# Kernel optimization log

Measured on AMD Instinct MI355X. Metric: run time of the kernel, lower is better.

Reference implementation:

```python
import jax, jax.numpy as jnp
import numpy as np

B, L, D_MODEL = 4, 2048, 2048
N_HEADS, HEAD_DIM = 16, 128
EPS = 1e-6


def _make_rope(key_unused, L, dim, base=10000.0):
    inv_freq = 1.0 / (base ** (np.arange(0, dim, 2, dtype=np.float32) / dim))  # [dim/2]
    t = np.arange(L, dtype=np.float32)
    freqs = np.outer(t, inv_freq)  # [L, dim/2]
    emb = np.concatenate([freqs, freqs], axis=-1)  # [L, dim]
    cos = np.broadcast_to(np.cos(emb)[None], (B, L, dim)).copy()
    sin = np.broadcast_to(np.sin(emb)[None], (B, L, dim)).copy()
    return jnp.asarray(cos), jnp.asarray(sin)


def setup_inputs() -> dict:
    key = jax.random.key(0)
    ks = jax.random.split(key, 8)
    s = 1.0 / np.sqrt(D_MODEL)
    x = jax.random.normal(ks[0], (B, L, D_MODEL), dtype=jnp.float32)
    cos_q, sin_q = _make_rope(None, L, HEAD_DIM)
    cos_k, sin_k = _make_rope(None, L, HEAD_DIM)
    Wq = jax.random.normal(ks[1], (D_MODEL, D_MODEL), dtype=jnp.float32) * s
    Wk = jax.random.normal(ks[2], (D_MODEL, D_MODEL), dtype=jnp.float32) * s
    Wv = jax.random.normal(ks[3], (D_MODEL, D_MODEL), dtype=jnp.float32) * s
    Wo = jax.random.normal(ks[4], (D_MODEL, D_MODEL), dtype=jnp.float32) * s
    q_gamma = jnp.ones((HEAD_DIM,), dtype=jnp.float32) + 0.02 * jax.random.normal(ks[5], (HEAD_DIM,), dtype=jnp.float32)
    k_gamma = jnp.ones((HEAD_DIM,), dtype=jnp.float32) + 0.02 * jax.random.normal(ks[6], (HEAD_DIM,), dtype=jnp.float32)
    return dict(x=x, cos_q=cos_q, sin_q=sin_q, cos_k=cos_k, sin_k=sin_k,
                Wq=Wq, Wk=Wk, Wv=Wv, Wo=Wo, q_gamma=q_gamma, k_gamma=k_gamma)


def _rms_norm(h, w):
    # T5-style RMSNorm over last dim (head_dim), variance in fp32
    var = jnp.mean(h.astype(jnp.float32) ** 2, axis=-1, keepdims=True)
    return w * (h * jax.lax.rsqrt(var + EPS))


def _rotate_half(x):
    d = x.shape[-1] // 2
    return jnp.concatenate([-x[..., d:], x[..., :d]], axis=-1)


def _apply_rope(x, cos, sin):
    # x: [B, L, H, Dh]; cos/sin: [B, L, Dh] -> broadcast over heads
    c = cos[:, :, None, :]
    s = sin[:, :, None, :]
    return x * c + _rotate_half(x) * s


def reference(x, cos_q, sin_q, cos_k, sin_k, Wq, Wk, Wv, Wo, q_gamma, k_gamma):
    Bx, Lx, _ = x.shape
    # QKV projections (Linear with weight [out, in]: y = x @ W.T)
    q = (x @ Wq.T).reshape(Bx, Lx, N_HEADS, HEAD_DIM)
    k = (x @ Wk.T).reshape(Bx, Lx, N_HEADS, HEAD_DIM)
    v = (x @ Wv.T).reshape(Bx, Lx, N_HEADS, HEAD_DIM)
    # per-head QK RMSNorm
    q = _rms_norm(q, q_gamma)
    k = _rms_norm(k, k_gamma)
    # dual RoPE
    q = _apply_rope(q, cos_q, sin_q)
    k = _apply_rope(k, cos_k, sin_k)
    # scaled dot-product attention (dense, no mask)
    scale = 1.0 / jnp.sqrt(jnp.asarray(HEAD_DIM, dtype=x.dtype))
    scores = jnp.einsum('blhd,bmhd->bhlm', q, k) * scale
    attn = jax.nn.softmax(scores, axis=-1)
    out = jnp.einsum('bhlm,bmhd->blhd', attn, v)
    out = out.reshape(Bx, Lx, N_HEADS * HEAD_DIM)
    return out @ Wo.T
```

## Files before the change

kernel.cpp:

```cpp
#include <hip/hip_runtime.h>
#include <stdint.h>

#define DM   2048
#define LSEQ 2048
#define NB   4
#define NH   16
#define HD   128
#define BL   (NB*LSEQ)

typedef unsigned short u16;
typedef short  short8 __attribute__((ext_vector_type(8)));
typedef float  f32x4  __attribute__((ext_vector_type(4)));
typedef float  f32x16 __attribute__((ext_vector_type(16)));

#define LOG2E 1.4426950408889634f

__device__ __forceinline__ float bf2f(u16 v) {
    union { unsigned u; float f; } x; x.u = ((unsigned)v) << 16; return x.f;
}
__device__ __forceinline__ u16 f2bf(float f) {
    union { float f; unsigned u; } x; x.f = f;
    return (u16)((x.u + 0x7FFF + ((x.u >> 16) & 1)) >> 16);
}

__device__ __forceinline__ short8 ld8(const void* base, size_t e, bool f32) {
    if (f32) {
        const float* p = (const float*)base + e;
        f32x4 a = *(const f32x4*)p;
        f32x4 b = *(const f32x4*)(p + 4);
        short8 r;
        #pragma unroll
        for (int i = 0; i < 4; ++i) { r[i] = (short)f2bf(a[i]); r[4+i] = (short)f2bf(b[i]); }
        return r;
    }
    return *(const short8*)((const u16*)base + e);
}
__device__ __forceinline__ float lde(const void* b, size_t e, bool f32) {
    return f32 ? ((const float*)b)[e] : bf2f(((const u16*)b)[e]);
}
__device__ __forceinline__ void st1(void* b, size_t e, float v, bool f32) {
    if (f32) ((float*)b)[e] = v; else ((u16*)b)[e] = f2bf(v);
}

extern "C" __global__ void dtype_probe(const u16* __restrict__ x, int* __restrict__ cnt) {
    int t = threadIdx.x;
    int insane = 0;
    #pragma unroll
    for (int j = 0; j < 16; ++j) {
        u16 u = x[t * 16 + j];
        int e = (u >> 7) & 0xFF;
        if (u != 0 && (e < 96 || e > 143)) insane++;
    }
    atomicAdd(cnt, insane);
}

extern "C" __global__ void to_bf16(const void* __restrict__ in, u16* __restrict__ out,
                                   int n8, const int* __restrict__ cnt)
{
    const bool isf = *cnt > 100;
    int i = blockIdx.x * 256 + threadIdx.x;
    if (i >= n8) return;
    *(short8*)(out + (size_t)i * 8) = ld8(in, (size_t)i * 8, isf);
}

__device__ __forceinline__ int swz128(int row, int col) {
    return row*128 + ((((col >> 3) ^ row) & 15) << 3) + (col & 7);
}
__device__ __forceinline__ int swz64(int row, int col) {
    return row*64 + ((((col >> 3) ^ row) & 7) << 3) + (col & 7);
}

typedef __attribute__((address_space(1))) const unsigned int guint;
typedef __attribute__((address_space(3))) unsigned int luint;
__device__ __forceinline__ void gl_lds16(const void* g, void* l) {
    __builtin_amdgcn_global_load_lds((guint*)g, (luint*)l, 16, 0, 0);
}

__device__ __forceinline__ void gemm_core_bf(const u16* __restrict__ A,
                                             const u16* __restrict__ W,
                                             u16* Al, u16* Bl,
                                             f32x4 acc[4][4],
                                             int m0, int n0, int t)
{
    const int lane = t & 63, w = t >> 6;
    const int quad = lane >> 4, l15 = lane & 15;
    const int wm = (w >> 1) * 64, wn = (w & 1) * 64;
    const int srow = w * 16 + (lane >> 2);
    const int scol = (lane & 3) * 8;
    const u16* ag = A + (size_t)(m0 + srow) * DM + scol;
    const u16* wg = W + (size_t)(n0 + srow) * DM + scol;
    u16* al0 = Al + (w * 16) * 32;
    u16* al1 = Al + (64 + w * 16) * 32;
    u16* bl0 = Bl + (w * 16) * 32;
    u16* bl1 = Bl + (64 + w * 16) * 32;

    for (int k0 = 0; k0 < DM; k0 += 32) {
        __syncthreads();
        gl_lds16(ag + k0,                   al0);
        gl_lds16(ag + k0 + (size_t)64 * DM, al1);
        gl_lds16(wg + k0,                   bl0);
        gl_lds16(wg + k0 + (size_t)64 * DM, bl1);
        __syncthreads();
        short8 afr[4], bfr[4];
        #pragma unroll
        for (int mt = 0; mt < 4; ++mt)
            afr[mt] = *(const short8*)&Al[(wm + mt*16 + l15)*32 + quad*8];
        #pragma unroll
        for (int nt = 0; nt < 4; ++nt)
            bfr[nt] = *(const short8*)&Bl[(wn + nt*16 + l15)*32 + quad*8];
        #pragma unroll
        for (int mt = 0; mt < 4; ++mt)
            #pragma unroll
            for (int nt = 0; nt < 4; ++nt)
                acc[mt][nt] = __builtin_amdgcn_mfma_f32_16x16x32_bf16(
                                  afr[mt], bfr[nt], acc[mt][nt], 0, 0, 0);
    }
}

extern "C" __global__ __launch_bounds__(256) void gemm_bf(
    const u16* __restrict__ A, const u16* __restrict__ W,
    void* __restrict__ O, const int* __restrict__ cnt, int o_sel)
{
    __shared__ __align__(16) u16 Al[128*32];
    __shared__ __align__(16) u16 Bl[128*32];
    const bool of = o_sel && (*cnt > 100);
    const int n0 = blockIdx.x * 128, m0 = blockIdx.y * 128;
    const int t = threadIdx.x, lane = t & 63, w = t >> 6;
    const int quad = lane >> 4, l15 = lane & 15;
    const int wm = (w >> 1) * 64, wn = (w & 1) * 64;

    f32x4 acc[4][4];
    #pragma unroll
    for (int i = 0; i < 4; ++i)
        #pragma unroll
        for (int j = 0; j < 4; ++j) acc[i][j] = (f32x4){0.f, 0.f, 0.f, 0.f};

    gemm_core_bf(A, W, Al, Bl, acc, m0, n0, t);

    #pragma unroll
    for (int mt = 0; mt < 4; ++mt)
        #pragma unroll
        for (int r = 0; r < 4; ++r) {
            size_t base = (size_t)(m0 + wm + mt*16 + quad*4 + r) * DM + n0 + wn + l15;
            #pragma unroll
            for (int nt = 0; nt < 4; ++nt) st1(O, base + nt*16, acc[mt][nt][r], of);
        }
}

extern "C" __global__ __launch_bounds__(256) void gemm_vb(
    const u16* __restrict__ A, const u16* __restrict__ W, u16* __restrict__ vT)
{
    __shared__ __align__(16) u16 Al[128*32];
    __shared__ __align__(16) u16 Bl[128*32];
    __shared__ __align__(16) u16 Tl[128*128];
    const int n0 = blockIdx.x * 128, m0 = blockIdx.y * 128;
    const int t = threadIdx.x, lane = t & 63, w = t >> 6;
    const int quad = lane >> 4, l15 = lane & 15;
    const int wm = (w >> 1) * 64, wn = (w & 1) * 64;

    f32x4 acc[4][4];
    #pragma unroll
    for (int i = 0; i < 4; ++i)
        #pragma unroll
        for (int j = 0; j < 4; ++j) acc[i][j] = (f32x4){0.f, 0.f, 0.f, 0.f};

    gemm_core_bf(A, W, Al, Bl, acc, m0, n0, t);

    #pragma unroll
    for (int mt = 0; mt < 4; ++mt)
        #pragma unroll
        for (int nt = 0; nt < 4; ++nt)
            #pragma unroll
            for (int r = 0; r < 4; ++r) {
                int m = wm + mt*16 + quad*4 + r;
                int n = wn + nt*16 + l15;
                Tl[swz128(n, m)] = f2bf(acc[mt][nt][r]);
            }
    __syncthreads();
    const int b  = m0 >> 11;
    const int l0 = m0 & (LSEQ - 1);
    #pragma unroll
    for (int it = 0; it < 8; ++it) {
        int c = t + 256*it;
        int nr = c >> 4, m8 = (c & 15) * 8;
        short8 val = *(const short8*)&Tl[swz128(nr, m8)];
        *(short8*)(vT + (size_t)b*DM*LSEQ + (size_t)(n0 + nr)*LSEQ + l0 + m8) = val;
    }
}

extern "C" __global__ void rmsrope(u16* __restrict__ q, u16* __restrict__ kk,
    const void* cq, const void* sq, const void* ck, const void* sk,
    const void* qg, const void* kg, const int* cnt)
{
    const bool isf = *cnt > 100;
    int t = blockIdx.x * 256 + threadIdx.x;
    int lane = t & 63;
    int widx = t >> 6;
    int h  = widx & (NH - 1);
    int bl = widx >> 4;
    size_t ro = (size_t)bl * DM + (size_t)h * HD;
    size_t co = (size_t)bl * HD;

    {
        float e0 = bf2f(q[ro + lane]), e1 = bf2f(q[ro + lane + 64]);
        float ss = e0*e0 + e1*e1;
        #pragma unroll
        for (int sm = 1; sm < 64; sm <<= 1) ss += __shfl_xor(ss, sm, 64);
        float r = rsqrtf(ss * (1.f / HD) + 1e-6f);
        float y0 = e0 * r * lde(qg, lane, isf);
        float y1 = e1 * r * lde(qg, lane + 64, isf);
        float c0 = lde(cq, co + lane, isf), c1 = lde(cq, co + lane + 64, isf);
        float s0 = lde(sq, co + lane, isf), s1 = lde(sq, co + lane + 64, isf);
        q[ro + lane]      = f2bf(y0 * c0 - y1 * s0);
        q[ro + lane + 64] = f2bf(y1 * c1 + y0 * s1);
    }
    {
        float e0 = bf2f(kk[ro + lane]), e1 = bf2f(kk[ro + lane + 64]);
        float ss = e0*e0 + e1*e1;
        #pragma unroll
        for (int sm = 1; sm < 64; sm <<= 1) ss += __shfl_xor(ss, sm, 64);
        float r = rsqrtf(ss * (1.f / HD) + 1e-6f);
        float y0 = e0 * r * lde(kg, lane, isf);
        float y1 = e1 * r * lde(kg, lane + 64, isf);
        float c0 = lde(ck, co + lane, isf), c1 = lde(ck, co + lane + 64, isf);
        float s0 = lde(sk, co + lane, isf), s1 = lde(sk, co + lane + 64, isf);
        kk[ro + lane]      = f2bf(y0 * c0 - y1 * s0);
        kk[ro + lane + 64] = f2bf(y1 * c1 + y0 * s1);
    }
}

extern "C" __global__ __launch_bounds__(256, 2) void flash(
    const u16* q, const u16* __restrict__ k,
    const u16* __restrict__ vT, u16* o)
{
    __shared__ __align__(16) u16 lds[17408];
    u16* Kl = lds;
    u16* Vl = lds + 8192;

    const int bh = blockIdx.x, b = bh >> 4, h = bh & 15;
    const int q0 = blockIdx.y * 128;
    const int t = threadIdx.x, lane = t & 63, w = t >> 6;
    const int l31 = lane & 31, hi8 = (lane >> 5) * 8;
    const size_t qko = (size_t)b * LSEQ * DM + (size_t)h * HD;
    const size_t vo  = (size_t)b * DM * LSEQ + (size_t)h * HD * LSEQ;

    short8 qf[8];
    #pragma unroll
    for (int ks = 0; ks < 8; ++ks)
        qf[ks] = *(const short8*)(q + qko +
                  (size_t)(q0 + w*32 + l31) * DM + ks*16 + hi8);

    f32x16 acc[4];
    f32x16 dacc;
    #pragma unroll
    for (int dt = 0; dt < 4; ++dt)
        #pragma unroll
        for (int r = 0; r < 16; ++r) acc[dt][r] = 0.f;
    #pragma unroll
    for (int r = 0; r < 16; ++r) dacc[r] = 0.f;
    float m2 = -30000.f;
    const float sl = 0.08838834764831845f * LOG2E;

    const short onev = (l31 == 0) ? (short)0x3F80 : (short)0;
    const short8 onesA = {onev, onev, onev, onev, onev, onev, onev, onev};

    const int krow = t >> 4,  kc8 = (t & 15) * 8;
    const int vrow = t >> 3,  vc8 = (t & 7) * 8;
    short8 kreg[4], vreg[4];
    #pragma unroll
    for (int it = 0; it < 4; ++it) {
        kreg[it] = *(const short8*)(k  + qko + (size_t)(krow + it*16) * DM + kc8);
        vreg[it] = *(const short8*)(vT + vo  + (size_t)(vrow + it*32) * LSEQ + vc8);
    }

    for (int kv0 = 0; kv0 < LSEQ; kv0 += 64) {
        __syncthreads();
        #pragma unroll
        for (int it = 0; it < 4; ++it) {
            *(short8*)&Kl[swz128(krow + it*16, kc8)] = kreg[it];
            *(short8*)&Vl[swz64 (vrow + it*32, vc8)] = vreg[it];
        }
        __syncthreads();
        if (kv0 + 64 < LSEQ) {
            #pragma unroll
            for (int it = 0; it < 4; ++it) {
                kreg[it] = *(const short8*)(k  + qko + (size_t)(kv0 + 64 + krow + it*16) * DM + kc8);
                vreg[it] = *(const short8*)(vT + vo  + (size_t)(vrow + it*32) * LSEQ + kv0 + 64 + vc8);
            }
        }

        f32x16 S0, S1;
        #pragma unroll
        for (int r = 0; r < 16; ++r) { S0[r] = 0.f; S1[r] = 0.f; }
        #pragma unroll
        for (int ks = 0; ks < 8; ++ks) {
            short8 kf0 = *(const short8*)&Kl[swz128(l31,      ks*16 + hi8)];
            short8 kf1 = *(const short8*)&Kl[swz128(32 + l31, ks*16 + hi8)];
            S0 = __builtin_amdgcn_mfma_f32_32x32x16_bf16(kf0, qf[ks], S0, 0, 0, 0);
            S1 = __builtin_amdgcn_mfma_f32_32x32x16_bf16(kf1, qf[ks], S1, 0, 0, 0);
        }

        float mv = fmaxf(S0[0], S1[0]);
        #pragma unroll
        for (int r = 1; r < 16; ++r) mv = fmaxf(mv, fmaxf(S0[r], S1[r]));
        mv = fmaxf(mv, __shfl_xor(mv, 32, 64));
        float msc = mv * sl;
        if (!__all(msc - m2 <= 8.0f)) {
            float mn = fmaxf(m2, msc);
            float al = exp2f(m2 - mn);
            m2 = mn;
            #pragma unroll
            for (int dt = 0; dt < 4; ++dt)
                #pragma unroll
                for (int r = 0; r < 16; ++r) acc[dt][r] *= al;
            dacc[0] *= al;
        }
        float p[32];
        #pragma unroll
        for (int r = 0; r < 16; ++r) p[r]      = exp2f(S0[r] * sl - m2);
        #pragma unroll
        for (int r = 0; r < 16; ++r) p[16 + r] = exp2f(S1[r] * sl - m2);

        #pragma unroll
        for (int kt = 0; kt < 2; ++kt) {
            unsigned pk[8];
            #pragma unroll
            for (int j = 0; j < 8; ++j)
                asm("v_cvt_pk_bf16_f32 %0, %1, %2"
                    : "=v"(pk[j]) : "v"(p[kt*16 + 2*j]), "v"(p[kt*16 + 2*j + 1]));
            asm volatile("v_permlane32_swap_b32 %0, %1" : "+v"(pk[0]), "+v"(pk[2]));
            asm volatile("v_permlane32_swap_b32 %0, %1" : "+v"(pk[1]), "+v"(pk[3]));
            asm volatile("v_permlane32_swap_b32 %0, %1" : "+v"(pk[4]), "+v"(pk[6]));
            asm volatile("v_permlane32_swap_b32 %0, %1" : "+v"(pk[5]), "+v"(pk[7]));
            union { unsigned u[4]; short8 v; } f0, f1;
            f0.u[0] = pk[0]; f0.u[1] = pk[1]; f0.u[2] = pk[2]; f0.u[3] = pk[3];
            f1.u[0] = pk[4]; f1.u[1] = pk[5]; f1.u[2] = pk[6]; f1.u[3] = pk[7];
            #pragma unroll
            for (int s = 0; s < 2; ++s) {
                short8 pf = s ? f1.v : f0.v;
                int slice = kt*2 + s;
                #pragma unroll
                for (int dt = 0; dt < 4; ++dt) {
                    short8 vf = *(const short8*)&Vl[swz64(dt*32 + l31, slice*16 + hi8)];
                    acc[dt] = __builtin_amdgcn_mfma_f32_32x32x16_bf16(vf, pf, acc[dt], 0, 0, 0);
                }
                dacc = __builtin_amdgcn_mfma_f32_32x32x16_bf16(onesA, pf, dacc, 0, 0, 0);
            }
        }
    }

    __syncthreads();
    u16* Ol = lds + w * 4352;
    float dn0 = dacc[0];
    float dnx = __shfl_xor(dn0, 32, 64);
    float inv = 1.f / ((lane & 32) ? dnx : dn0);
    #pragma unroll
    for (int dt = 0; dt < 4; ++dt)
        #pragma unroll
        for (int i = 0; i < 8; ++i) {
            float a0 = acc[dt][2*i]     * inv;
            float a1 = acc[dt][2*i + 1] * inv;
            unsigned pkv;
            asm("v_cvt_pk_bf16_f32 %0, %1, %2" : "=v"(pkv) : "v"(a0), "v"(a1));
            int d = dt*32 + ((i & 1) << 1) + ((i >> 1) << 3) + ((lane >> 5) << 2);
            *(unsigned*)&Ol[l31*136 + d] = pkv;
        }
    __syncthreads();
    #pragma unroll
    for (int j = 0; j < 8; ++j) {
        int cb = (lane >> 5) + 2*j;
        short8 vv = *(const short8*)&Ol[l31*136 + cb*8];
        *(short8*)(o + qko + (size_t)(q0 + w*32 + l31) * DM + cb*8) = vv;
    }
}

extern "C" void kernel_launch(void* const* d_in, const int* in_sizes, int n_in,
                              void* d_out, int out_size, void* d_ws, size_t ws_size,
                              hipStream_t stream)
{
    const void* x  = d_in[0];
    const void* cq = d_in[1];
    const void* sq = d_in[2];
    const void* ck = d_in[3];
    const void* sk = d_in[4];
    const void* Wq = d_in[5];
    const void* Wk = d_in[6];
    const void* Wv = d_in[7];
    const void* Wo = d_in[8];
    const void* qg = d_in[9];
    const void* kg = d_in[10];

    u16* qws = (u16*)d_ws;
    u16* kws = qws + (size_t)BL * DM;
    u16* vtw = kws + (size_t)BL * DM;
    u16* wsl = vtw + (size_t)BL * DM;
    int* cnt = (int*)(wsl + (size_t)DM * DM);
    u16* xb  = (u16*)d_out;

    const int xn8 = BL * DM / 8;
    const int wn8 = DM * DM / 8;

    hipMemsetAsync(cnt, 0, 4, stream);
    dtype_probe<<<1, 256, 0, stream>>>((const u16*)x, cnt);

    to_bf16<<<xn8 / 256, 256, 0, stream>>>(x, xb, xn8, cnt);

    to_bf16<<<wn8 / 256, 256, 0, stream>>>(Wv, wsl, wn8, cnt);
    gemm_vb<<<dim3(16, 64), 256, 0, stream>>>(xb, wsl, vtw);

    to_bf16<<<wn8 / 256, 256, 0, stream>>>(Wq, wsl, wn8, cnt);
    gemm_bf<<<dim3(16, 64), 256, 0, stream>>>(xb, wsl, qws, cnt, 0);

    to_bf16<<<wn8 / 256, 256, 0, stream>>>(Wk, wsl, wn8, cnt);
    gemm_bf<<<dim3(16, 64), 256, 0, stream>>>(xb, wsl, kws, cnt, 0);

    rmsrope<<<dim3(BL * NH / 4), 256, 0, stream>>>(qws, kws, cq, sq, ck, sk, qg, kg, cnt);

    flash<<<dim3(64, 16), 256, 0, stream>>>(qws, kws, vtw, qws);

    to_bf16<<<wn8 / 256, 256, 0, stream>>>(Wo, wsl, wn8, cnt);
    gemm_bf<<<dim3(16, 64), 256, 0, stream>>>(qws, wsl, d_out, cnt, 1);
}
```

Baseline: 816.9 us.

## Double-buffer flash K/V tiles, batch weight casts and fuse Q/K projection launches

The flash kernel now keeps two LDS buffers for K/V tiles. It prefetches two tiles ahead so there is one barrier per iteration instead of two, and it raises wave priority with s_setprio around the MFMA sections. On the host side, the four weight conversions are merged into a single launch that writes four separate workspace buffers. The Q and K projection GEMMs are merged into one grid using a z dimension. This cuts the number of kernel launches and serial dependencies, at the cost of more LDS per flash block (64KB), which may lower occupancy against the requested two blocks per CU, and a larger workspace.

Result: faster. 773.1 us (-5.4%).

```diff
diff --git a/kernel.cpp b/kernel.cpp
--- a/kernel.cpp
+++ b/kernel.cpp
@@ -60,6 +60,24 @@
     const bool isf = *cnt > 100;
     int i = blockIdx.x * 256 + threadIdx.x;
     if (i >= n8) return;
+    *(short8*)(out + (size_t)i * 8) = ld8(in, (size_t)i * 8, isf);
+}
+
+extern "C" __global__ void to_bf16_w(const void* w0, const void* w1,
+                                     const void* w2, const void* w3,
+                                     u16* o0, u16* o1, u16* o2, u16* o3,
+                                     int n8, const int* __restrict__ cnt)
+{
+    const bool isf = *cnt > 100;
+    int i = blockIdx.x * 256 + threadIdx.x;
+    if (i >= n8) return;
+    const void* in; u16* out;
+    switch (blockIdx.y) {
+        case 0:  in = w0; out = o0; break;
+        case 1:  in = w1; out = o1; break;
+        case 2:  in = w2; out = o2; break;
+        default: in = w3; out = o3; break;
+    }
     *(short8*)(out + (size_t)i * 8) = ld8(in, (size_t)i * 8, isf);
 }
 
@@ -147,6 +165,37 @@
         }
 }
 
+extern "C" __global__ __launch_bounds__(256) void gemm_qk2(
+    const u16* __restrict__ A, const u16* __restrict__ W0, const u16* __restrict__ W1,
+    u16* __restrict__ O0, u16* __restrict__ O1)
+{
+    __shared__ __align__(16) u16 Al[128*32];
+    __shared__ __align__(16) u16 Bl[128*32];
+    const u16* W = blockIdx.z ? W1 : W0;
+    u16*       O = blockIdx.z ? O1 : O0;
+    const int n0 = blockIdx.x * 128, m0 = blockIdx.y * 128;
+    const int t = threadIdx.x, lane = t & 63, w = t >> 6;
+    const int quad = lane >> 4, l15 = lane & 15;
+    const int wm = (w >> 1) * 64, wn = (w & 1) * 64;
+
+    f32x4 acc[4][4];
+    #pragma unroll
+    for (int i = 0; i < 4; ++i)
+        #pragma unroll
+        for (int j = 0; j < 4; ++j) acc[i][j] = (f32x4){0.f, 0.f, 0.f, 0.f};
+
+    gemm_core_bf(A, W, Al, Bl, acc, m0, n0, t);
+
+    #pragma unroll
+    for (int mt = 0; mt < 4; ++mt)
+        #pragma unroll
+        for (int r = 0; r < 4; ++r) {
+            size_t base = (size_t)(m0 + wm + mt*16 + quad*4 + r) * DM + n0 + wn + l15;
+            #pragma unroll
+            for (int nt = 0; nt < 4; ++nt) O[base + nt*16] = f2bf(acc[mt][nt][r]);
+        }
+}
+
 extern "C" __global__ __launch_bounds__(256) void gemm_vb(
     const u16* __restrict__ A, const u16* __restrict__ W, u16* __restrict__ vT)
 {
@@ -233,9 +282,7 @@
     const u16* q, const u16* __restrict__ k,
     const u16* __restrict__ vT, u16* o)
 {
-    __shared__ __align__(16) u16 lds[17408];
-    u16* Kl = lds;
-    u16* Vl = lds + 8192;
+    __shared__ __align__(16) u16 lds[32768];
 
     const int bh = blockIdx.x, b = bh >> 4, h = bh & 15;
     const int q0 = blockIdx.y * 128;
@@ -250,14 +297,14 @@
         qf[ks] = *(const short8*)(q + qko +
                   (size_t)(q0 + w*32 + l31) * DM + ks*16 + hi8);
 
+    f32x16 zz;
+    #pragma unroll
+    for (int r = 0; r < 16; ++r) zz[r] = 0.f;
     f32x16 acc[4];
     f32x16 dacc;
     #pragma unroll
-    for (int dt = 0; dt < 4; ++dt)
-        #pragma unroll
-        for (int r = 0; r < 16; ++r) acc[dt][r] = 0.f;
-    #pragma unroll
-    for (int r = 0; r < 16; ++r) dacc[r] = 0.f;
+    for (int dt = 0; dt < 4; ++dt) acc[dt] = zz;
+    dacc = zz;
     float m2 = -30000.f;
     const float sl = 0.08838834764831845f * LOG2E;
 
@@ -267,38 +314,66 @@
     const int krow = t >> 4,  kc8 = (t & 15) * 8;
     const int vrow = t >> 3,  vc8 = (t & 7) * 8;
     short8 kreg[4], vreg[4];
+
     #pragma unroll
     for (int it = 0; it < 4; ++it) {
         kreg[it] = *(const short8*)(k  + qko + (size_t)(krow + it*16) * DM + kc8);
         vreg[it] = *(const short8*)(vT + vo  + (size_t)(vrow + it*32) * LSEQ + vc8);
     }
-
-    for (int kv0 = 0; kv0 < LSEQ; kv0 += 64) {
-        __syncthreads();
+    {
+        u16* Kn = lds;  u16* Vn = lds + 8192;
         #pragma unroll
         for (int it = 0; it < 4; ++it) {
-            *(short8*)&Kl[swz128(krow + it*16, kc8)] = kreg[it];
-            *(short8*)&Vl[swz64 (vrow + it*32, vc8)] = vreg[it];
-        }
-        __syncthreads();
-        if (kv0 + 64 < LSEQ) {
+            *(short8*)&Kn[swz128(krow + it*16, kc8)] = kreg[it];
+            *(short8*)&Vn[swz64 (vrow + it*32, vc8)] = vreg[it];
+        }
+    }
+    #pragma unroll
+    for (int it = 0; it < 4; ++it) {
+        kreg[it] = *(const short8*)(k  + qko + (size_t)(64 + krow + it*16) * DM + kc8);
+        vreg[it] = *(const short8*)(vT + vo  + (size_t)(vrow + it*32) * LSEQ + 64 + vc8);
+    }
+    __syncthreads();
+
+    const int NT = LSEQ / 64;
+    for (int it0 = 0; it0 < NT; ++it0) {
+        const int cur = it0 & 1;
+        if (it0 + 1 < NT) {
+            u16* Kn = lds + (cur ^ 1) * 16384;
+            u16* Vn = Kn + 8192;
             #pragma unroll
             for (int it = 0; it < 4; ++it) {
-                kreg[it] = *(const short8*)(k  + qko + (size_t)(kv0 + 64 + krow + it*16) * DM + kc8);
-                vreg[it] = *(const short8*)(vT + vo  + (size_t)(vrow + it*32) * LSEQ + kv0 + 64 + vc8);
+                *(short8*)&Kn[swz128(krow + it*16, kc8)] = kreg[it];
+                *(short8*)&Vn[swz64 (vrow + it*32, vc8)] = vreg[it];
             }
         }
+        if (it0 + 2 < NT) {
+            const int kv = (it0 + 2) * 64;
+            #pragma unroll
+            for (int it = 0; it < 4; ++it) {
+                kreg[it] = *(const short8*)(k  + qko + (size_t)(kv + krow + it*16) * DM + kc8);
+                vreg[it] = *(const short8*)(vT + vo  + (size_t)(vrow + it*32) * LSEQ + kv + vc8);
+            }
+        }
+        u16* Kl = lds + cur * 16384;
+        u16* Vl = Kl + 8192;
 
         f32x16 S0, S1;
-        #pragma unroll
-        for (int r = 0; r < 16; ++r) { S0[r] = 0.f; S1[r] = 0.f; }
-        #pragma unroll
-        for (int ks = 0; ks < 8; ++ks) {
+        __builtin_amdgcn_s_setprio(1);
+        {
+            short8 kf0 = *(const short8*)&Kl[swz128(l31,      hi8)];
+            short8 kf1 = *(const short8*)&Kl[swz128(32 + l31, hi8)];
+            S0 = __builtin_amdgcn_mfma_f32_32x32x16_bf16(kf0, qf[0], zz, 0, 0, 0);
+            S1 = __builtin_amdgcn_mfma_f32_32x32x16_bf16(kf1, qf[0], zz, 0, 0, 0);
+        }
+        #pragma unroll
+        for (int ks = 1; ks < 8; ++ks) {
             short8 kf0 = *(const short8*)&Kl[swz128(l31,      ks*16 + hi8)];
             short8 kf1 = *(const short8*)&Kl[swz128(32 + l31, ks*16 + hi8)];
             S0 = __builtin_amdgcn_mfma_f32_32x32x16_bf16(kf0, qf[ks], S0, 0, 0, 0);
             S1 = __builtin_amdgcn_mfma_f32_32x32x16_bf16(kf1, qf[ks], S1, 0, 0, 0);
         }
+        __builtin_amdgcn_s_setprio(0);
 
         float mv = fmaxf(S0[0], S1[0]);
         #pragma unroll
@@ -339,17 +414,19 @@
             for (int s = 0; s < 2; ++s) {
                 short8 pf = s ? f1.v : f0.v;
                 int slice = kt*2 + s;
+                __builtin_amdgcn_s_setprio(1);
                 #pragma unroll
                 for (int dt = 0; dt < 4; ++dt) {
                     short8 vf = *(const short8*)&Vl[swz64(dt*32 + l31, slice*16 + hi8)];
                     acc[dt] = __builtin_amdgcn_mfma_f32_32x32x16_bf16(vf, pf, acc[dt], 0, 0, 0);
                 }
                 dacc = __builtin_amdgcn_mfma_f32_32x32x16_bf16(onesA, pf, dacc, 0, 0, 0);
+                __builtin_amdgcn_s_setprio(0);
             }
         }
-    }
-
-    __syncthreads();
+        __syncthreads();
+    }
+
     u16* Ol = lds + w * 4352;
     float dn0 = dacc[0];
     float dnx = __shfl_xor(dn0, 32, 64);
@@ -393,8 +470,11 @@
     u16* qws = (u16*)d_ws;
     u16* kws = qws + (size_t)BL * DM;
     u16* vtw = kws + (size_t)BL * DM;
-    u16* wsl = vtw + (size_t)BL * DM;
-    int* cnt = (int*)(wsl + (size_t)DM * DM);
+    u16* wqs = vtw + (size_t)BL * DM;
+    u16* wks = wqs + (size_t)DM * DM;
+    u16* wvs = wks + (size_t)DM * DM;
+    u16* wos = wvs + (size_t)DM * DM;
+    int* cnt = (int*)(wos + (size_t)DM * DM);
     u16* xb  = (u16*)d_out;
 
     const int xn8 = BL * DM / 8;
@@ -404,20 +484,15 @@
     dtype_probe<<<1, 256, 0, stream>>>((const u16*)x, cnt);
 
     to_bf16<<<xn8 / 256, 256, 0, stream>>>(x, xb, xn8, cnt);
-
-    to_bf16<<<wn8 / 256, 256, 0, stream>>>(Wv, wsl, wn8, cnt);
-    gemm_vb<<<dim3(16, 64), 256, 0, stream>>>(xb, wsl, vtw);
-
-    to_bf16<<<wn8 / 256, 256, 0, stream>>>(Wq, wsl, wn8, cnt);
-    gemm_bf<<<dim3(16, 64), 256, 0, stream>>>(xb, wsl, qws, cnt, 0);
-
-    to_bf16<<<wn8 / 256, 256, 0, stream>>>(Wk, wsl, wn8, cnt);
-    gemm_bf<<<dim3(16, 64), 256, 0, stream>>>(xb, wsl, kws, cnt, 0);
+    to_bf16_w<<<dim3(wn8 / 256, 4), 256, 0, stream>>>(Wq, Wk, Wv, Wo,
+                                                      wqs, wks, wvs, wos, wn8, cnt);
+
+    gemm_vb <<<dim3(16, 64),    256, 0, stream>>>(xb, wvs, vtw);
+    gemm_qk2<<<dim3(16, 64, 2), 256, 0, stream>>>(xb, wqs, wks, qws, kws);
 
     rmsrope<<<dim3(BL * NH / 4), 256, 0, stream>>>(qws, kws, cq, sq, ck, sk, qg, kg, cnt);
 
     flash<<<dim3(64, 16), 256, 0, stream>>>(qws, kws, vtw, qws);
 
-    to_bf16<<<wn8 / 256, 256, 0, stream>>>(Wo, wsl, wn8, cnt);
-    gemm_bf<<<dim3(16, 64), 256, 0, stream>>>(qws, wsl, d_out, cnt, 1);
-}
+    gemm_bf<<<dim3(16, 64), 256, 0, stream>>>(qws, wos, d_out, cnt, 1);
+}
```
